# Kernel tuning notes

Measured on AMD Instinct MI355X. Metric: run time of the kernel, lower is better.

Reference implementation:

```python
import jax, jax.numpy as jnp
import numpy as np
from jax.scipy.special import logsumexp

L = 5          # label_size (fixed by label2idx)
START = 3
END = 4
PAD = 2
NEG = -10000.0


def setup_inputs() -> dict:
    B, S = 4096, 512
    key = jax.random.key(0)
    k1, k2, k3, k4 = jax.random.split(key, 4)
    lstm_scores = jax.random.normal(k1, (B, S, L), dtype=jnp.float32)
    transition = jax.random.normal(k2, (L, L), dtype=jnp.float32)
    transition = (transition.at[:, START].set(NEG)
                            .at[END, :].set(NEG)
                            .at[:, PAD].set(NEG)
                            .at[PAD, :].set(NEG))
    word_seq_lens = jax.random.randint(k3, (B,), 1, S + 1)  # lengths in [1, S]
    tags = jax.random.randint(k4, (B, S), 0, 2)             # gold labels in {0,1}
    mask = jnp.arange(S)[None, :] < word_seq_lens[:, None]   # (B, S) bool
    return {"lstm_scores": lstm_scores, "transition": transition,
            "word_seq_lens": word_seq_lens, "tags": tags, "mask": mask}


def reference(lstm_scores, transition, word_seq_lens, tags, mask):
    B, S, _ = lstm_scores.shape
    # all_scores[b,t,i,j] = transition[i,j] + emission[b,t,j]  -> (B,S,L,L)
    all_scores = transition[None, None, :, :] + lstm_scores[:, :, None, :]

    # ---- forward algorithm (normalizer) via scan over time ----
    alpha0 = all_scores[:, 0, START, :]              # (B, L)
    scores_t = jnp.swapaxes(all_scores, 0, 1)        # (S, B, L, L)

    def step(alpha, sc_t):
        new = logsumexp(alpha[:, :, None] + sc_t, axis=1)  # (B, L)
        return new, new

    _, alphas = jax.lax.scan(step, alpha0, scores_t[1:])   # (S-1, B, L)
    alphas = jnp.concatenate([alpha0[None], alphas], axis=0)  # (S, B, L)
    alphas = jnp.swapaxes(alphas, 0, 1)                       # (B, S, L)

    idx = jnp.broadcast_to((word_seq_lens - 1)[:, None, None], (B, 1, L))
    last_alpha = jnp.take_along_axis(alphas, idx, axis=1)[:, 0, :]  # (B, L)
    last_alpha = last_alpha + transition[:, END][None, :]
    unlabeled = jnp.sum(logsumexp(last_alpha, axis=1))

    # ---- gold path score ----
    tag_idx = jnp.broadcast_to(tags[:, :, None, None], (B, S, L, 1))
    cur = jnp.take_along_axis(all_scores, tag_idx, axis=3)[..., 0]  # (B, S, L)
    middle = jnp.take_along_axis(cur[:, 1:, :], tags[:, :-1, None], axis=2)[..., 0]  # (B, S-1)
    begin = cur[:, 0, START]
    end_ids = jnp.take_along_axis(tags, (word_seq_lens - 1)[:, None], axis=1)[:, 0]
    end_sc = transition[end_ids, END]
    labeled = (jnp.sum(begin) + jnp.sum(end_sc)
               + jnp.sum(jnp.where(mask[:, 1:], middle, 0.0)))

    return unlabeled, labeled
```

## Files before the change

kernel.cpp:

```cpp
#include <hip/hip_runtime.h>


__device__ __forceinline__ void rescale4(float& a, float& b, float& c, float& d,
                                         float& logZ) {
    float m = fmaxf(fmaxf(a, b), fmaxf(c, d));
    int k = (__float_as_int(m) >> 23) & 0xFF;
    float scale = __int_as_float((254 - k) << 23);
    logZ += (float)(k - 127) * 0.69314718055994530942f;
    a *= scale; b *= scale; c *= scale; d *= scale;
}

template <int SG>
__global__ __launch_bounds__(256) void crf_fwd_wave(
    const float* __restrict__ lstm,
    const float* __restrict__ trans,
    const int* __restrict__ lens,
    const int* __restrict__ tags,
    float* __restrict__ out,
    int B, int S, int SgDyn) {
    const int lane = threadIdx.x & 63;
    const int wid = threadIdx.x >> 6;
    const int nw = blockDim.x >> 6;
    const int b = blockIdx.x * nw + wid;
    const bool valid = (b < B);

    const float T00 = trans[0], T01 = trans[1];
    const float T04 = trans[4];
    const float T10 = trans[5], T11 = trans[6];
    const float T14 = trans[9];
    const float T30 = trans[15], T31 = trans[16];
    const float E00 = __expf(T00), E01 = __expf(T01);
    const float E10 = __expf(T10), E11 = __expf(T11);

    const int len = valid ? lens[b] : 0;
    const float* __restrict__ xrow = lstm + (size_t)b * S * 5;
    const int* __restrict__ trow = tags + (size_t)b * S;

    const int Sg = (SG > 0) ? SG : SgDyn;
    const int tA = 1 + lane * Sg;
    const int tB = min(tA + Sg, len);

    float m00 = 1.f, m01 = 0.f, m10 = 0.f, m11 = 1.f;
    float logZ = 0.f;
    float lab = 0.f;

    if (tA < len) {
        int prev = trow[tA - 1] & 1;
#pragma unroll
        for (int u = 0; u < Sg; ++u) {
            int t = tA + u;
            if (t < tB) {
                float x0 = xrow[t * 5 + 0];
                float x1 = xrow[t * 5 + 1];
                int tg = trow[t] & 1;
                float ex0 = __expf(x0), ex1 = __expf(x1);
                float n00 = E00 * ex0, n01 = E10 * ex0;
                float n10 = E01 * ex1, n11 = E11 * ex1;
                float r00 = fmaf(n00, m00, n01 * m10);
                float r01 = fmaf(n00, m01, n01 * m11);
                float r10 = fmaf(n10, m00, n11 * m10);
                float r11 = fmaf(n10, m01, n11 * m11);
                m00 = r00; m01 = r01; m10 = r10; m11 = r11;
                int idx = (prev << 1) | tg;
                float Tpt = (idx == 0) ? T00 : (idx == 1) ? T01
                                         : (idx == 2) ? T10 : T11;
                lab += Tpt + (tg ? x1 : x0);
                if (t == len - 1) lab += tg ? T14 : T04;
                prev = tg;
            }
            if ((u & 3) == 3) rescale4(m00, m01, m10, m11, logZ);
        }
        rescale4(m00, m01, m10, m11, logZ);
    }

#pragma unroll
    for (int msk = 1; msk < 64; msk <<= 1) {
        float o00 = __shfl_xor(m00, msk);
        float o01 = __shfl_xor(m01, msk);
        float o10 = __shfl_xor(m10, msk);
        float o11 = __shfl_xor(m11, msk);
        float oz = __shfl_xor(logZ, msk);
        float ol = __shfl_xor(lab, msk);
        const bool upper = (lane & msk) != 0;
        float a00 = upper ? m00 : o00, a01 = upper ? m01 : o01;
        float a10 = upper ? m10 : o10, a11 = upper ? m11 : o11;
        float c00 = upper ? o00 : m00, c01 = upper ? o01 : m01;
        float c10 = upper ? o10 : m10, c11 = upper ? o11 : m11;
        m00 = fmaf(a00, c00, a01 * c10);
        m01 = fmaf(a00, c01, a01 * c11);
        m10 = fmaf(a10, c00, a11 * c10);
        m11 = fmaf(a10, c01, a11 * c11);
        logZ += oz;
        lab += ol;
        rescale4(m00, m01, m10, m11, logZ);
    }

    __shared__ float red[2][8];
    float unlab_w = 0.f, lab_w = 0.f;
    if (lane == 0 && valid) {
        float x00 = xrow[0], x01 = xrow[1];
        int tg0 = trow[0] & 1;
        float p0 = __expf(T30 + x00);
        float p1 = __expf(T31 + x01);
        float f0 = fmaf(m00, p0, m01 * p1);
        float f1 = fmaf(m10, p0, m11 * p1);
        float s = fmaf(f0, __expf(T04), f1 * __expf(T14));
        unlab_w = logZ + __logf(s);
        lab_w = lab + (tg0 ? T31 + x01 : T30 + x00);
        if (len == 1) lab_w += tg0 ? T14 : T04;
    }
    if (lane == 0) {
        red[0][wid] = unlab_w;
        red[1][wid] = lab_w;
    }
    __syncthreads();
    if (threadIdx.x == 0) {
        float su = 0.f, sl = 0.f;
        for (int w = 0; w < nw; ++w) {
            su += red[0][w];
            sl += red[1][w];
        }
        atomicAdd(&out[0], su);
        atomicAdd(&out[1], sl);
    }
}

extern "C" void kernel_launch(void* const* d_in, const int* in_sizes, int n_in,
                              void* d_out, int out_size, void* d_ws, size_t ws_size,
                              hipStream_t stream) {
    const float* lstm = (const float*)d_in[0];
    const float* trans = (const float*)d_in[1];
    const int* lens = (const int*)d_in[2];
    const int* tags = (const int*)d_in[3];
    float* out = (float*)d_out;

    const int B = in_sizes[2];
    const int S = in_sizes[3] / B;
    const int Sg = (S - 1 + 63) >> 6;

    hipMemsetAsync(out, 0, out_size * sizeof(float), stream);
    const int ROWS_PER_BLOCK = 4;
    dim3 block(64 * ROWS_PER_BLOCK);
    dim3 grid((B + ROWS_PER_BLOCK - 1) / ROWS_PER_BLOCK);
    if (Sg == 8) {
        crf_fwd_wave<8><<<grid, block, 0, stream>>>(lstm, trans, lens, tags, out, B, S, Sg);
    } else {
        crf_fwd_wave<0><<<grid, block, 0, stream>>>(lstm, trans, lens, tags, out, B, S, Sg);
    }
}
```

Before: 121.4 us.

## Stage each row's emissions and tags into LDS with coalesced float4 loads

For S=512, each wave first copies its row's emission scores and tags into shared memory with coalesced 16-byte loads, reading only up to the row's valid length. Lanes then read their strided 8-step chunks from LDS instead of doing scattered 20-byte-stride global reads. Blocks shrink to 2 waves so the roughly 14 KB of LDS per block still allows reasonable occupancy. The cost is an extra block barrier and LDS traffic, and LDS bank conflicts from the stride-40 per-lane access pattern.

```diff
diff --git a/kernel.cpp b/kernel.cpp
--- a/kernel.cpp
+++ b/kernel.cpp
@@ -1,5 +1,7 @@
 #include <hip/hip_runtime.h>
 
+
+#define ROWS 2
 
 __device__ __forceinline__ void rescale4(float& a, float& b, float& c, float& d,
                                          float& logZ) {
@@ -10,19 +12,46 @@
     a *= scale; b *= scale; c *= scale; d *= scale;
 }
 
-template <int SG>
-__global__ __launch_bounds__(256) void crf_fwd_wave(
+template <int S, int SG>
+__global__ __launch_bounds__(64 * ROWS) void crf_fwd_staged(
     const float* __restrict__ lstm,
     const float* __restrict__ trans,
     const int* __restrict__ lens,
     const int* __restrict__ tags,
     float* __restrict__ out,
-    int B, int S, int SgDyn) {
+    int B) {
+    __shared__ float4 xs4[ROWS][S * 5 / 4];
+    __shared__ int4 tg4[ROWS][S / 4];
+    __shared__ float red[2][ROWS];
+
     const int lane = threadIdx.x & 63;
     const int wid = threadIdx.x >> 6;
-    const int nw = blockDim.x >> 6;
-    const int b = blockIdx.x * nw + wid;
+    const int b = blockIdx.x * ROWS + wid;
     const bool valid = (b < B);
+    const int len = valid ? lens[b] : 0;
+
+    if (valid) {
+        const float4* __restrict__ src =
+            reinterpret_cast<const float4*>(lstm + (size_t)b * S * 5);
+        const int nf4 = (len * 5 + 3) >> 2;
+#pragma unroll
+        for (int i = 0; i < S * 5 / 4 / 64; ++i) {
+            int j = lane + 64 * i;
+            if (j < nf4) xs4[wid][j] = src[j];
+        }
+        const int4* __restrict__ tsrc =
+            reinterpret_cast<const int4*>(tags + (size_t)b * S);
+        const int nt4 = (len + 3) >> 2;
+#pragma unroll
+        for (int i = 0; i < S / 4 / 64; ++i) {
+            int j = lane + 64 * i;
+            if (j < nt4) tg4[wid][j] = tsrc[j];
+        }
+    }
+    __syncthreads();
+
+    const float* __restrict__ xr = reinterpret_cast<const float*>(xs4[wid]);
+    const int* __restrict__ tr = reinterpret_cast<const int*>(tg4[wid]);
 
     const float T00 = trans[0], T01 = trans[1];
     const float T04 = trans[4];
@@ -32,21 +61,124 @@
     const float E00 = __expf(T00), E01 = __expf(T01);
     const float E10 = __expf(T10), E11 = __expf(T11);
 
+    const int tA = 1 + lane * SG;
+    const int tB = min(tA + SG, len);
+
+    float m00 = 1.f, m01 = 0.f, m10 = 0.f, m11 = 1.f;
+    float logZ = 0.f;
+    float lab = 0.f;
+
+    if (tA < len) {
+        int prev = tr[tA - 1] & 1;
+#pragma unroll
+        for (int u = 0; u < SG; ++u) {
+            int t = tA + u;
+            if (t < tB) {
+                float x0 = xr[t * 5 + 0];
+                float x1 = xr[t * 5 + 1];
+                int tg = tr[t] & 1;
+                float ex0 = __expf(x0), ex1 = __expf(x1);
+                float n00 = E00 * ex0, n01 = E10 * ex0;
+                float n10 = E01 * ex1, n11 = E11 * ex1;
+                float r00 = fmaf(n00, m00, n01 * m10);
+                float r01 = fmaf(n00, m01, n01 * m11);
+                float r10 = fmaf(n10, m00, n11 * m10);
+                float r11 = fmaf(n10, m01, n11 * m11);
+                m00 = r00; m01 = r01; m10 = r10; m11 = r11;
+                int idx = (prev << 1) | tg;
+                float Tpt = (idx == 0) ? T00 : (idx == 1) ? T01
+                                         : (idx == 2) ? T10 : T11;
+                lab += Tpt + (tg ? x1 : x0);
+                if (t == len - 1) lab += tg ? T14 : T04;
+                prev = tg;
+            }
+            if ((u & 3) == 3) rescale4(m00, m01, m10, m11, logZ);
+        }
+        rescale4(m00, m01, m10, m11, logZ);
+    }
+
+#pragma unroll
+    for (int msk = 1; msk < 64; msk <<= 1) {
+        float o00 = __shfl_xor(m00, msk);
+        float o01 = __shfl_xor(m01, msk);
+        float o10 = __shfl_xor(m10, msk);
+        float o11 = __shfl_xor(m11, msk);
+        float oz = __shfl_xor(logZ, msk);
+        float ol = __shfl_xor(lab, msk);
+        const bool upper = (lane & msk) != 0;
+        float a00 = upper ? m00 : o00, a01 = upper ? m01 : o01;
+        float a10 = upper ? m10 : o10, a11 = upper ? m11 : o11;
+        float c00 = upper ? o00 : m00, c01 = upper ? o01 : m01;
+        float c10 = upper ? o10 : m10, c11 = upper ? o11 : m11;
+        m00 = fmaf(a00, c00, a01 * c10);
+        m01 = fmaf(a00, c01, a01 * c11);
+        m10 = fmaf(a10, c00, a11 * c10);
+        m11 = fmaf(a10, c01, a11 * c11);
+        logZ += oz;
+        lab += ol;
+        rescale4(m00, m01, m10, m11, logZ);
+    }
+
+    float unlab_w = 0.f, lab_w = 0.f;
+    if (lane == 0 && valid) {
+        float x00 = xr[0], x01 = xr[1];
+        int tg0 = tr[0] & 1;
+        float p0 = __expf(T30 + x00);
+        float p1 = __expf(T31 + x01);
+        float f0 = fmaf(m00, p0, m01 * p1);
+        float f1 = fmaf(m10, p0, m11 * p1);
+        float s = fmaf(f0, __expf(T04), f1 * __expf(T14));
+        unlab_w = logZ + __logf(s);
+        lab_w = lab + (tg0 ? T31 + x01 : T30 + x00);
+        if (len == 1) lab_w += tg0 ? T14 : T04;
+    }
+    if (lane == 0) {
+        red[0][wid] = unlab_w;
+        red[1][wid] = lab_w;
+    }
+    __syncthreads();
+    if (threadIdx.x == 0) {
+        float su = 0.f, sl = 0.f;
+#pragma unroll
+        for (int w = 0; w < ROWS; ++w) {
+            su += red[0][w];
+            sl += red[1][w];
+        }
+        atomicAdd(&out[0], su);
+        atomicAdd(&out[1], sl);
+    }
+}
+
+__global__ __launch_bounds__(256) void crf_fwd_wave_gen(
+    const float* __restrict__ lstm, const float* __restrict__ trans,
+    const int* __restrict__ lens, const int* __restrict__ tags,
+    float* __restrict__ out, int B, int S, int Sg) {
+    const int lane = threadIdx.x & 63;
+    const int wid = threadIdx.x >> 6;
+    const int nw = blockDim.x >> 6;
+    const int b = blockIdx.x * nw + wid;
+    const bool valid = (b < B);
+
+    const float T00 = trans[0], T01 = trans[1];
+    const float T04 = trans[4];
+    const float T10 = trans[5], T11 = trans[6];
+    const float T14 = trans[9];
+    const float T30 = trans[15], T31 = trans[16];
+    const float E00 = __expf(T00), E01 = __expf(T01);
+    const float E10 = __expf(T10), E11 = __expf(T11);
+
     const int len = valid ? lens[b] : 0;
     const float* __restrict__ xrow = lstm + (size_t)b * S * 5;
     const int* __restrict__ trow = tags + (size_t)b * S;
 
-    const int Sg = (SG > 0) ? SG : SgDyn;
     const int tA = 1 + lane * Sg;
     const int tB = min(tA + Sg, len);
 
     float m00 = 1.f, m01 = 0.f, m10 = 0.f, m11 = 1.f;
-    float logZ = 0.f;
-    float lab = 0.f;
+    float logZ = 0.f, lab = 0.f;
 
     if (tA < len) {
         int prev = trow[tA - 1] & 1;
-#pragma unroll
         for (int u = 0; u < Sg; ++u) {
             int t = tA + u;
             if (t < tB) {
@@ -136,15 +268,18 @@
 
     const int B = in_sizes[2];
     const int S = in_sizes[3] / B;
-    const int Sg = (S - 1 + 63) >> 6;
 
     hipMemsetAsync(out, 0, out_size * sizeof(float), stream);
-    const int ROWS_PER_BLOCK = 4;
-    dim3 block(64 * ROWS_PER_BLOCK);
-    dim3 grid((B + ROWS_PER_BLOCK - 1) / ROWS_PER_BLOCK);
-    if (Sg == 8) {
-        crf_fwd_wave<8><<<grid, block, 0, stream>>>(lstm, trans, lens, tags, out, B, S, Sg);
+    if (S == 512) {
+        dim3 block(64 * ROWS);
+        dim3 grid((B + ROWS - 1) / ROWS);
+        crf_fwd_staged<512, 8><<<grid, block, 0, stream>>>(lstm, trans, lens,
+                                                           tags, out, B);
     } else {
-        crf_fwd_wave<0><<<grid, block, 0, stream>>>(lstm, trans, lens, tags, out, B, S, Sg);
-    }
-}
+        const int Sg = (S - 1 + 63) >> 6;
+        dim3 block(256);
+        dim3 grid((B + 3) / 4);
+        crf_fwd_wave_gen<<<grid, block, 0, stream>>>(lstm, trans, lens, tags,
+                                                     out, B, S, Sg);
+    }
+}
```

After: 143.2 us. 18.0% more time.
